# Kernel tuning notes

Measured on AMD Instinct MI355X. Metric: run time of the kernel, lower is better.

Reference implementation:

```python
import jax, jax.numpy as jnp
import numpy as np
from jax import lax

# LIF parameters (norse defaults)
DT = 0.001
TAU_SYN_INV = 200.0
TAU_MEM_INV = 100.0
V_TH = 1.0
V_LEAK = 0.0
V_RESET = 0.0


def _spike(v_minus_th):
    # forward heaviside (surrogate grad only matters for bwd module)
    return (v_minus_th > 0).astype(v_minus_th.dtype)


def setup_inputs() -> dict:
    key = jax.random.key(0)
    ks = jax.random.split(key, 5)
    B, T, F, H, O = 256, 1000, 128, 256, 2
    x = jax.random.normal(ks[0], (B, T, F), dtype=jnp.float32)
    w_in = jax.random.normal(ks[1], (H, F), dtype=jnp.float32) / np.sqrt(F)
    w_rec = jax.random.normal(ks[2], (H, H), dtype=jnp.float32) / np.sqrt(H)
    fc_w = jax.random.normal(ks[3], (O, H), dtype=jnp.float32) / np.sqrt(H)
    fc_b = jnp.zeros((O,), dtype=jnp.float32)
    return {"x": x, "w_in": w_in, "w_rec": w_rec, "fc_w": fc_w, "fc_b": fc_b}


def reference(x, w_in, w_rec, fc_w, fc_b):
    B = x.shape[0]
    H = w_in.shape[0]
    # precompute feed-forward input currents for all timesteps: [B,T,H] -> [T,B,H]
    xw = jnp.einsum("btf,hf->bth", x, w_in)
    xw = jnp.swapaxes(xw, 0, 1)

    def step(carry, xt):
        v, i, z = carry
        # membrane decay toward leak + synaptic current integration
        v_dec = v + DT * TAU_MEM_INV * ((V_LEAK - v) + i)
        # synaptic current decay
        i_dec = i * (1.0 - DT * TAU_SYN_INV)
        # threshold / spike / reset
        z_new = _spike(v_dec - V_TH)
        v_new = (1.0 - z_new) * v_dec + z_new * V_RESET
        # inject feed-forward + recurrent current for next step
        i_new = i_dec + xt + z @ w_rec.T
        return (v_new, i_new, z_new), z_new

    zeros = jnp.zeros((B, H), dtype=x.dtype)
    _, zs = lax.scan(step, (zeros, zeros, zeros), xw)  # zs: [T,B,H]
    total_activity = zs.sum(axis=0)  # sum over time (torch dim=1 batch-first)
    return total_activity @ fc_w.T + fc_b
```

## Files before the change

kernel.cpp:

```cpp
#include <hip/hip_runtime.h>
#include <hip/hip_bf16.h>
#include <stdint.h>

constexpr int B = 256, T = 1000, F = 128, H = 256, O = 2;
constexpr float DT_TAU_MEM = 0.1f;
constexpr float SYN_DECAY  = 0.8f;
constexpr float V_THRESH   = 1.0f;

__device__ inline unsigned short f2bf_raw(float f) {
  __hip_bfloat16 b = __float2bfloat16(f);
  return *reinterpret_cast<unsigned short*>(&b);
}

template <typename XT> struct XConv;
template <> struct XConv<float> {
  static __device__ inline float load(const float* p) { return *p; }
  static __device__ inline void store4(float* p, float a, float b, float c, float d) {
    *reinterpret_cast<float4*>(p) = make_float4(a, b, c, d);
  }
};
template <> struct XConv<__hip_bfloat16> {
  static __device__ inline float load(const __hip_bfloat16* p) { return __bfloat162float(*p); }
  static __device__ inline void store4(__hip_bfloat16* p, float a, float b, float c, float d) {
    ushort4 u = make_ushort4(f2bf_raw(a), f2bf_raw(b), f2bf_raw(c), f2bf_raw(d));
    *reinterpret_cast<ushort4*>(p) = u;
  }
};

__global__ void transpose_wrec(const float* __restrict__ w, float* __restrict__ wT) {
  int k = blockIdx.x;
  int h = threadIdx.x;
  wT[k * H + h] = w[h * H + k];
}

template <typename XT>
__global__ __launch_bounds__(256) void gemm_xw(const float* __restrict__ x,
                                               const float* __restrict__ w_in,
                                               XT* __restrict__ xw) {
  constexpr int K = 128;
  constexpr int SA = 68;
  __shared__ float As[K][SA];
  __shared__ float Bs[K][SA];

  const int m0 = blockIdx.x * 64;
  const int n0 = blockIdx.y * 64;
  const int tid = threadIdx.x;

  {
    const int r  = tid >> 2;
    const int cq = tid & 3;
    const float* xa = x    + (size_t)(m0 + r) * K;
    const float* xb = w_in + (size_t)(n0 + r) * K;
#pragma unroll
    for (int j = 0; j < 8; ++j) {
      const int c = (cq + (j << 2)) << 2;
      float4 av = *reinterpret_cast<const float4*>(xa + c);
      float4 bv = *reinterpret_cast<const float4*>(xb + c);
      As[c + 0][r] = av.x; As[c + 1][r] = av.y; As[c + 2][r] = av.z; As[c + 3][r] = av.w;
      Bs[c + 0][r] = bv.x; Bs[c + 1][r] = bv.y; Bs[c + 2][r] = bv.z; Bs[c + 3][r] = bv.w;
    }
  }
  __syncthreads();

  const int tn = (tid & 15) << 2;
  const int tm = (tid >> 4) << 2;
  float acc[4][4] = {};

#pragma unroll 16
  for (int k = 0; k < K; ++k) {
    float4 a = *reinterpret_cast<const float4*>(&As[k][tm]);
    float4 b = *reinterpret_cast<const float4*>(&Bs[k][tn]);
    acc[0][0] += a.x * b.x; acc[0][1] += a.x * b.y; acc[0][2] += a.x * b.z; acc[0][3] += a.x * b.w;
    acc[1][0] += a.y * b.x; acc[1][1] += a.y * b.y; acc[1][2] += a.y * b.z; acc[1][3] += a.y * b.w;
    acc[2][0] += a.z * b.x; acc[2][1] += a.z * b.y; acc[2][2] += a.z * b.z; acc[2][3] += a.z * b.w;
    acc[3][0] += a.w * b.x; acc[3][1] += a.w * b.y; acc[3][2] += a.w * b.z; acc[3][3] += a.w * b.w;
  }

#pragma unroll
  for (int im = 0; im < 4; ++im) {
    XT* p = xw + (size_t)(m0 + tm + im) * H + (n0 + tn);
    XConv<XT>::store4(p, acc[im][0], acc[im][1], acc[im][2], acc[im][3]);
  }
}

template <typename XT>
__global__ __launch_bounds__(256) void scan_lif(const XT* __restrict__ xw,
                                                const float* __restrict__ wT,
                                                const float* __restrict__ fc_w,
                                                const float* __restrict__ fc_b,
                                                float* __restrict__ out) {
  const int b = blockIdx.x;
  const int h = threadIdx.x;

  __shared__ int   spk[2][H];
  __shared__ int   cnt[2];
  __shared__ float red[8];

  if (h < 2) cnt[h] = 0;
  __syncthreads();

  float v = 0.f, cur = 0.f;
  int spike_count = 0;

  const XT* xrow = xw + (size_t)b * T * H + h;
  float x0 = XConv<XT>::load(xrow);
  float x1 = XConv<XT>::load(xrow + H);

  for (int t = 0; t < T; ++t) {
    const int cb = t & 1, nb = cb ^ 1;
    const float xt = x0;
    x0 = x1;
    x1 = (t + 2 < T) ? XConv<XT>::load(xrow + (size_t)(t + 2) * H) : 0.f;

    float rec = 0.f;
    const int c = cnt[cb];
    int j = 0;
    for (; j + 4 <= c; j += 4) {
      const int k0 = spk[cb][j + 0], k1 = spk[cb][j + 1];
      const int k2 = spk[cb][j + 2], k3 = spk[cb][j + 3];
      const float w0 = wT[(k0 << 8) + h];
      const float w1 = wT[(k1 << 8) + h];
      const float w2 = wT[(k2 << 8) + h];
      const float w3 = wT[(k3 << 8) + h];
      rec += (w0 + w1) + (w2 + w3);
    }
    for (; j < c; ++j) rec += wT[(spk[cb][j] << 8) + h];

    const float v_dec = v + DT_TAU_MEM * (cur - v);
    const int z = v_dec > V_THRESH;
    v = z ? 0.f : v_dec;
    cur = cur * SYN_DECAY + xt + rec;
    spike_count += z;

    __syncthreads();
    if (z) { int p = atomicAdd(&cnt[nb], 1); spk[nb][p] = h; }
    if (h == 0) cnt[cb] = 0;
    __syncthreads();
  }

  const float cf = (float)spike_count;
#pragma unroll
  for (int o = 0; o < O; ++o) {
    float p = cf * fc_w[o * H + h];
#pragma unroll
    for (int off = 32; off > 0; off >>= 1) p += __shfl_down(p, off, 64);
    if ((h & 63) == 0) red[o * 4 + (h >> 6)] = p;
    __syncthreads();
  }
  if (h < O) {
    out[b * O + h] = (red[h * 4 + 0] + red[h * 4 + 1] + red[h * 4 + 2] + red[h * 4 + 3]) + fc_b[h];
  }
}

extern "C" void kernel_launch(void* const* d_in, const int* in_sizes, int n_in,
                              void* d_out, int out_size, void* d_ws, size_t ws_size,
                              hipStream_t stream) {
  const float* x     = (const float*)d_in[0];
  const float* w_in  = (const float*)d_in[1];
  const float* w_rec = (const float*)d_in[2];
  const float* fc_w  = (const float*)d_in[3];
  const float* fc_b  = (const float*)d_in[4];
  float* out = (float*)d_out;

  float* wT = (float*)d_ws;
  const size_t wT_bytes = (size_t)H * H * sizeof(float);
  char* xw_base = (char*)d_ws + wT_bytes;
  const size_t xw_elems = (size_t)B * T * H;
  const bool use_f32 = ws_size >= wT_bytes + xw_elems * sizeof(float);

  transpose_wrec<<<H, H, 0, stream>>>(w_rec, wT);

  if (use_f32) {
    float* xw = (float*)xw_base;
    gemm_xw<float><<<dim3(B * T / 64, H / 64), 256, 0, stream>>>(x, w_in, xw);
    scan_lif<float><<<B, H, 0, stream>>>(xw, wT, fc_w, fc_b, out);
  } else {
    __hip_bfloat16* xw = (__hip_bfloat16*)xw_base;
    gemm_xw<__hip_bfloat16><<<dim3(B * T / 64, H / 64), 256, 0, stream>>>(x, w_in, xw);
    scan_lif<__hip_bfloat16><<<B, H, 0, stream>>>(xw, wT, fc_w, fc_b, out);
  }
}
```

Before: 1.172 ms.

## Replace sparse spike gather in LIF scan with split-fp16 MFMA recurrent matmul

The scan kernel now processes 16 batch rows per block and computes the recurrent current as a dense spike-matrix times w_rec product using fp16 MFMA instructions. w_rec is held in registers as a scaled high/low fp16 pair so the result stays close to fp32. Spikes are exchanged through a double-buffered shared fp16 matrix, replacing the atomic spike-list gather, and the separate transpose kernel is removed. The aim is to drop per-step gather latency and use matrix cores. The cost is dense work regardless of spike sparsity, only 16 blocks on the GPU, and heavy register use.

After: 1.598 ms. 1.36x slower.

```diff
diff --git a/kernel.cpp b/kernel.cpp
--- a/kernel.cpp
+++ b/kernel.cpp
@@ -7,6 +7,9 @@
 constexpr float SYN_DECAY  = 0.8f;
 constexpr float V_THRESH   = 1.0f;
 
+typedef __attribute__((ext_vector_type(8))) _Float16 half8v;
+typedef __attribute__((ext_vector_type(4))) float f32x4;
+
 __device__ inline unsigned short f2bf_raw(float f) {
   __hip_bfloat16 b = __float2bfloat16(f);
   return *reinterpret_cast<unsigned short*>(&b);
@@ -14,24 +17,31 @@
 
 template <typename XT> struct XConv;
 template <> struct XConv<float> {
-  static __device__ inline float load(const float* p) { return *p; }
+  typedef float4 Raw;
+  static __device__ inline Raw loadraw(const float* p) {
+    return *reinterpret_cast<const float4*>(p);
+  }
+  static __device__ inline float extract(const Raw& r, int i) {
+    return reinterpret_cast<const float*>(&r)[i];
+  }
   static __device__ inline void store4(float* p, float a, float b, float c, float d) {
     *reinterpret_cast<float4*>(p) = make_float4(a, b, c, d);
   }
 };
 template <> struct XConv<__hip_bfloat16> {
-  static __device__ inline float load(const __hip_bfloat16* p) { return __bfloat162float(*p); }
+  typedef ushort4 Raw;
+  static __device__ inline Raw loadraw(const __hip_bfloat16* p) {
+    return *reinterpret_cast<const ushort4*>(p);
+  }
+  static __device__ inline float extract(const Raw& r, int i) {
+    unsigned u = reinterpret_cast<const unsigned short*>(&r)[i];
+    return __uint_as_float(u << 16);
+  }
   static __device__ inline void store4(__hip_bfloat16* p, float a, float b, float c, float d) {
     ushort4 u = make_ushort4(f2bf_raw(a), f2bf_raw(b), f2bf_raw(c), f2bf_raw(d));
     *reinterpret_cast<ushort4*>(p) = u;
   }
 };
-
-__global__ void transpose_wrec(const float* __restrict__ w, float* __restrict__ wT) {
-  int k = blockIdx.x;
-  int h = threadIdx.x;
-  wT[k * H + h] = w[h * H + k];
-}
 
 template <typename XT>
 __global__ __launch_bounds__(256) void gemm_xw(const float* __restrict__ x,
@@ -83,72 +93,143 @@
   }
 }
 
+
 template <typename XT>
-__global__ __launch_bounds__(256) void scan_lif(const XT* __restrict__ xw,
-                                                const float* __restrict__ wT,
-                                                const float* __restrict__ fc_w,
-                                                const float* __restrict__ fc_b,
-                                                float* __restrict__ out) {
-  const int b = blockIdx.x;
-  const int h = threadIdx.x;
-
-  __shared__ int   spk[2][H];
-  __shared__ int   cnt[2];
-  __shared__ float red[8];
-
-  if (h < 2) cnt[h] = 0;
+__global__ __launch_bounds__(256, 1) void scan_lif(const XT* __restrict__ xw,
+                                                   const float* __restrict__ w_rec,
+                                                   const float* __restrict__ fc_w,
+                                                   const float* __restrict__ fc_b,
+                                                   float* __restrict__ out) {
+  const int tid = threadIdx.x;
+  const int w  = tid >> 6;
+  const int l  = tid & 63;
+  const int lg = l & 15;
+  const int lk = l >> 4;
+  const int g0 = blockIdx.x * 16;
+
+  __shared__ unsigned short Zb[2][16][264];
+  __shared__ float red[16][2];
+
+  {
+    unsigned* p = reinterpret_cast<unsigned*>(&Zb[0][0][0]);
+    for (int i = tid; i < (int)(sizeof(Zb) / 4); i += 256) p[i] = 0u;
+  }
+  if (tid < 32) (&red[0][0])[tid] = 0.f;
+
+  half8v afr_h[4][8], afr_m[4][8];
+#pragma unroll
+  for (int rt = 0; rt < 4; ++rt) {
+    const float* wrow = w_rec + (size_t)(64 * w + 16 * rt + lg) * H + 8 * lk;
+#pragma unroll
+    for (int ks = 0; ks < 8; ++ks) {
+      half8v fh, fm;
+#pragma unroll
+      for (int e = 0; e < 8; ++e) {
+        const float ws = wrow[32 * ks + e] * 1024.f;
+        const _Float16 h = (_Float16)ws;
+        const float r = ws - (float)h;
+        fh[e] = h;
+        fm[e] = (_Float16)(r * 4096.f);
+      }
+      afr_h[rt][ks] = fh;
+      afr_m[rt][ks] = fm;
+    }
+  }
+
+  float v[16], cur[16];
+  int   cnt[16];
+#pragma unroll
+  for (int i = 0; i < 16; ++i) { v[i] = 0.f; cur[i] = 0.f; cnt[i] = 0; }
+
+  const XT* xb = xw + (size_t)(g0 + lg) * T * H + 64 * w + 4 * lk;
+
+  typename XConv<XT>::Raw xr0[4], xr1[4];
+#pragma unroll
+  for (int rt = 0; rt < 4; ++rt) xr0[rt] = XConv<XT>::loadraw(xb + 0 * H + 16 * rt);
+#pragma unroll
+  for (int rt = 0; rt < 4; ++rt) xr1[rt] = XConv<XT>::loadraw(xb + 1 * H + 16 * rt);
+
   __syncthreads();
 
-  float v = 0.f, cur = 0.f;
-  int spike_count = 0;
-
-  const XT* xrow = xw + (size_t)b * T * H + h;
-  float x0 = XConv<XT>::load(xrow);
-  float x1 = XConv<XT>::load(xrow + H);
-
-  for (int t = 0; t < T; ++t) {
-    const int cb = t & 1, nb = cb ^ 1;
-    const float xt = x0;
-    x0 = x1;
-    x1 = (t + 2 < T) ? XConv<XT>::load(xrow + (size_t)(t + 2) * H) : 0.f;
-
-    float rec = 0.f;
-    const int c = cnt[cb];
-    int j = 0;
-    for (; j + 4 <= c; j += 4) {
-      const int k0 = spk[cb][j + 0], k1 = spk[cb][j + 1];
-      const int k2 = spk[cb][j + 2], k3 = spk[cb][j + 3];
-      const float w0 = wT[(k0 << 8) + h];
-      const float w1 = wT[(k1 << 8) + h];
-      const float w2 = wT[(k2 << 8) + h];
-      const float w3 = wT[(k3 << 8) + h];
-      rec += (w0 + w1) + (w2 + w3);
-    }
-    for (; j < c; ++j) rec += wT[(spk[cb][j] << 8) + h];
-
-    const float v_dec = v + DT_TAU_MEM * (cur - v);
-    const int z = v_dec > V_THRESH;
-    v = z ? 0.f : v_dec;
-    cur = cur * SYN_DECAY + xt + rec;
-    spike_count += z;
-
-    __syncthreads();
-    if (z) { int p = atomicAdd(&cnt[nb], 1); spk[nb][p] = h; }
-    if (h == 0) cnt[cb] = 0;
-    __syncthreads();
-  }
-
-  const float cf = (float)spike_count;
-#pragma unroll
-  for (int o = 0; o < O; ++o) {
-    float p = cf * fc_w[o * H + h];
-#pragma unroll
-    for (int off = 32; off > 0; off >>= 1) p += __shfl_down(p, off, 64);
-    if ((h & 63) == 0) red[o * 4 + (h >> 6)] = p;
-    __syncthreads();
-  }
-  if (h < O) {
-    out[b * O + h] = (red[h * 4 + 0] + red[h * 4 + 1] + red[h * 4 + 2] + red[h * 4 + 3]) + fc_b[h];
+#define LSTEP(XR, RD, WR) do {                                                 \
+    f32x4 ach[4], acm[4];                                                      \
+    _Pragma("unroll")                                                          \
+    for (int rt = 0; rt < 4; ++rt) {                                           \
+      ach[rt] = (f32x4){0.f, 0.f, 0.f, 0.f};                                   \
+      acm[rt] = (f32x4){0.f, 0.f, 0.f, 0.f};                                   \
+    }                                                                          \
+    _Pragma("unroll")                                                          \
+    for (int ksg = 0; ksg < 2; ++ksg) {                                        \
+      half8v bf[4];                                                            \
+      _Pragma("unroll")                                                        \
+      for (int k2 = 0; k2 < 4; ++k2)                                           \
+        bf[k2] = *reinterpret_cast<const half8v*>(                             \
+            &Zb[RD][lg][32 * (4 * ksg + k2) + 8 * lk]);                        \
+      _Pragma("unroll")                                                        \
+      for (int k2 = 0; k2 < 4; ++k2) {                                         \
+        const int ks = 4 * ksg + k2;                                           \
+        _Pragma("unroll")                                                      \
+        for (int rt = 0; rt < 4; ++rt) {                                       \
+          ach[rt] = __builtin_amdgcn_mfma_f32_16x16x32_f16(afr_h[rt][ks],      \
+                        bf[k2], ach[rt], 0, 0, 0);                             \
+          acm[rt] = __builtin_amdgcn_mfma_f32_16x16x32_f16(afr_m[rt][ks],      \
+                        bf[k2], acm[rt], 0, 0, 0);                             \
+        }                                                                      \
+      }                                                                        \
+    }                                                                          \
+    _Pragma("unroll")                                                          \
+    for (int rt = 0; rt < 4; ++rt) {                                           \
+      ushort4 zw;                                                              \
+      _Pragma("unroll")                                                        \
+      for (int r = 0; r < 4; ++r) {                                            \
+        const int i = rt * 4 + r;                                              \
+        const float rec = (ach[rt][r] + acm[rt][r] * (1.f / 4096.f))           \
+                          * (1.f / 1024.f);                                    \
+        const float xt = XConv<XT>::extract(XR[rt], r);                        \
+        const float vd = v[i] + DT_TAU_MEM * (cur[i] - v[i]);                  \
+        const int z = vd > V_THRESH;                                           \
+        v[i] = z ? 0.f : vd;                                                   \
+        cur[i] = cur[i] * SYN_DECAY + xt + rec;                                \
+        cnt[i] += z;                                                           \
+        reinterpret_cast<unsigned short*>(&zw)[r] = z ? 0x3C00u : 0u;          \
+      }                                                                        \
+      *reinterpret_cast<ushort4*>(&Zb[WR][lg][64 * w + 16 * rt + 4 * lk]) = zw; \
+    }                                                                          \
+    __syncthreads();                                                           \
+  } while (0)
+
+  for (int j = 0; j < 500; ++j) {
+    LSTEP(xr0, 0, 1);
+    {
+      const size_t t2 = (2 * j + 2 < T) ? (size_t)(2 * j + 2) : (size_t)(T - 1);
+#pragma unroll
+      for (int rt = 0; rt < 4; ++rt) xr0[rt] = XConv<XT>::loadraw(xb + t2 * H + 16 * rt);
+    }
+    LSTEP(xr1, 1, 0);
+    {
+      const size_t t3 = (2 * j + 3 < T) ? (size_t)(2 * j + 3) : (size_t)(T - 1);
+#pragma unroll
+      for (int rt = 0; rt < 4; ++rt) xr1[rt] = XConv<XT>::loadraw(xb + t3 * H + 16 * rt);
+    }
+  }
+#undef LSTEP
+
+  float po0 = 0.f, po1 = 0.f;
+#pragma unroll
+  for (int rt = 0; rt < 4; ++rt)
+#pragma unroll
+    for (int r = 0; r < 4; ++r) {
+      const int h = 64 * w + 16 * rt + 4 * lk + r;
+      const float c = (float)cnt[rt * 4 + r];
+      po0 += c * fc_w[h];
+      po1 += c * fc_w[H + h];
+    }
+  atomicAdd(&red[lg][0], po0);
+  atomicAdd(&red[lg][1], po1);
+  __syncthreads();
+  if (tid < 32) {
+    const int g = tid >> 1, o = tid & 1;
+    out[(size_t)(g0 + g) * O + o] = red[g][o] + fc_b[o];
   }
 }
 
@@ -162,21 +243,16 @@
   const float* fc_b  = (const float*)d_in[4];
   float* out = (float*)d_out;
 
-  float* wT = (float*)d_ws;
-  const size_t wT_bytes = (size_t)H * H * sizeof(float);
-  char* xw_base = (char*)d_ws + wT_bytes;
   const size_t xw_elems = (size_t)B * T * H;
-  const bool use_f32 = ws_size >= wT_bytes + xw_elems * sizeof(float);
-
-  transpose_wrec<<<H, H, 0, stream>>>(w_rec, wT);
+  const bool use_f32 = ws_size >= xw_elems * sizeof(float);
 
   if (use_f32) {
-    float* xw = (float*)xw_base;
+    float* xw = (float*)d_ws;
     gemm_xw<float><<<dim3(B * T / 64, H / 64), 256, 0, stream>>>(x, w_in, xw);
-    scan_lif<float><<<B, H, 0, stream>>>(xw, wT, fc_w, fc_b, out);
+    scan_lif<float><<<B / 16, 256, 0, stream>>>(xw, w_rec, fc_w, fc_b, out);
   } else {
-    __hip_bfloat16* xw = (__hip_bfloat16*)xw_base;
+    __hip_bfloat16* xw = (__hip_bfloat16*)d_ws;
     gemm_xw<__hip_bfloat16><<<dim3(B * T / 64, H / 64), 256, 0, stream>>>(x, w_in, xw);
-    scan_lif<__hip_bfloat16><<<B, H, 0, stream>>>(xw, wT, fc_w, fc_b, out);
-  }
-}
+    scan_lif<__hip_bfloat16><<<B / 16, 256, 0, stream>>>(xw, w_rec, fc_w, fc_b, out);
+  }
+}
```
